# Kernel optimization log

Measured on AMD Instinct MI355X. Metric: run time of the kernel, lower is better.

Reference implementation:

```python
import jax, jax.numpy as jnp
import numpy as np

N = 100000      # nodes
E = 1600000     # edges (before self-loops)
IN = 128        # in_size
H = 4           # heads
C = 32          # out_size // heads
OUT = H * C     # 128
NEG_SLOPE = 0.2
LN_EPS = 1e-5
SM_EPS = 1e-16  # PyG softmax eps


def setup_inputs() -> dict:
    key = jax.random.key(0)
    ks = jax.random.split(key, 6)
    x = jax.random.normal(ks[0], (N, IN), dtype=jnp.float32)
    edge_index = jax.random.randint(ks[1], (2, E), 0, N, dtype=jnp.int64)
    W = jax.random.normal(ks[2], (IN, OUT), dtype=jnp.float32) * 0.05
    a_src = jax.random.normal(ks[3], (H, C), dtype=jnp.float32) * 0.05
    a_dst = jax.random.normal(ks[4], (H, C), dtype=jnp.float32) * 0.05
    bias = jnp.zeros((OUT,), dtype=jnp.float32)
    gamma = jnp.ones((OUT,), dtype=jnp.float32)
    beta = jnp.zeros((OUT,), dtype=jnp.float32)
    return {"x": x, "edge_index": edge_index, "W": W, "a_src": a_src,
            "a_dst": a_dst, "bias": bias, "gamma": gamma, "beta": beta}


def reference(x, edge_index, W, a_src, a_dst, bias, gamma, beta):
    n = x.shape[0]
    # add self loops (PyG GATConv default)
    loops = jnp.arange(n, dtype=edge_index.dtype)
    src = jnp.concatenate([edge_index[0], loops])  # [E+N]
    dst = jnp.concatenate([edge_index[1], loops])

    h = (x @ W).reshape(n, H, C)                   # [N,H,C]
    alpha_src = jnp.sum(h * a_src, axis=-1)        # [N,H]
    alpha_dst = jnp.sum(h * a_dst, axis=-1)        # [N,H]

    e = jax.nn.leaky_relu(alpha_src[src] + alpha_dst[dst], NEG_SLOPE)  # [E+N,H]
    # segment softmax over edges grouped by destination node
    emax = jax.ops.segment_max(e, dst, num_segments=n)
    emax = jnp.where(jnp.isfinite(emax), emax, 0.0)
    ee = jnp.exp(e - emax[dst])
    denom = jax.ops.segment_sum(ee, dst, num_segments=n)
    alpha = ee / (denom[dst] + SM_EPS)             # [E+N,H]

    msg = h[src] * alpha[:, :, None]               # [E+N,H,C]
    out = jax.ops.segment_sum(msg, dst, num_segments=n).reshape(n, OUT) + bias

    # LayerNorm(out_size)
    mu = jnp.mean(out, axis=-1, keepdims=True)
    var = jnp.var(out, axis=-1, keepdims=True)
    out = (out - mu) * jax.lax.rsqrt(var + LN_EPS) * gamma + beta
    return jax.nn.relu(out)
```

## Files before the change

### kernel.cpp

```cpp
#include <hip/hip_runtime.h>
#include <hip/hip_bf16.h>
#include <math.h>

#define IN_DIM 128
#define OUT_DIM 128
#define NHEAD 4
#define HC 32
#define NEG_SLOPE 0.2f
#define LN_EPS 1e-5f
#define SM_EPS 1e-16f

#define NB_SHIFT 9
#define BDST 512
#define NBUCK_MAX 256
#define BIN_ITER 28
#define BIN_CHUNK (BIN_ITER * 256)
#define SRC_BITS 17
#define SRC_MASK ((1u << SRC_BITS) - 1u)
#define BCAP_SHIFT 14
#define BCAP (1 << BCAP_SHIFT)

typedef __attribute__((ext_vector_type(8))) short bf16x8;
typedef __attribute__((ext_vector_type(4))) short short4v;
typedef __attribute__((ext_vector_type(4))) float f32x4;

__device__ __forceinline__ float leaky(float v) { return v > 0.f ? v : NEG_SLOPE * v; }

__device__ __forceinline__ short f2b(float f) {
    __hip_bfloat16 b = __float2bfloat16(f);
    return *reinterpret_cast<short*>(&b);
}
__device__ __forceinline__ float b2f(short s) {
    return __uint_as_float(((unsigned)(unsigned short)s) << 16);
}

__device__ __forceinline__ int swz(int row, int byteInRow) {
    return row * 256 + (byteInRow ^ ((row & 7) << 4));
}

__global__ void k_prepW(const float* __restrict__ W, __hip_bfloat16* __restrict__ WtB,
                        int* __restrict__ bcur)
{
    int t0 = blockIdx.x * 256 + threadIdx.x;
    int k = t0 >> 7, j = t0 & 127;
    WtB[j * IN_DIM + k] = __float2bfloat16(W[t0]);
    if (blockIdx.x == 0) bcur[threadIdx.x] = 0;
}

__global__ void __launch_bounds__(256)
k_gemm_bin(const float* __restrict__ x, const __hip_bfloat16* __restrict__ WtB,
           const float* __restrict__ a_src, const float* __restrict__ a_dst,
           __hip_bfloat16* __restrict__ hB, float* __restrict__ asrc_out,
           float* __restrict__ adst_out,
           const int* __restrict__ ei, int* __restrict__ bcur,
           unsigned* __restrict__ binned,
           int E, int N, int nblk_bin)
{
    __shared__ __align__(16) char lds[32768];
    const int t = threadIdx.x;

    if ((int)blockIdx.x < nblk_bin) {
        int* cnt = (int*)lds;
        int* gb  = (int*)(lds + 1024);
        int tot = E + N;
        int base = (int)blockIdx.x * BIN_CHUNK;

        cnt[t] = 0;
        __syncthreads();

        int rk[BIN_ITER], bk[BIN_ITER], dlo[BIN_ITER];
        #pragma unroll
        for (int k = 0; k < BIN_ITER; ++k) {
            int e = base + k * 256 + t;
            bk[k] = -1; rk[k] = 0; dlo[k] = 0;
            if (e < tot) {
                int d = (e < E) ? ei[E + e] : (e - E);
                bk[k] = d >> NB_SHIFT;
                dlo[k] = d & (BDST - 1);
                rk[k] = atomicAdd(&cnt[bk[k]], 1);
            }
        }
        __syncthreads();
        gb[t] = cnt[t] ? ((t << BCAP_SHIFT) + atomicAdd(&bcur[t], cnt[t])) : 0;
        __syncthreads();
        #pragma unroll
        for (int k = 0; k < BIN_ITER; ++k) {
            int e = base + k * 256 + t;
            if (e < tot) {
                int s = (e < E) ? ei[e] : (e - E);
                binned[gb[bk[k]] + rk[k]] = (unsigned)s | ((unsigned)dlo[k] << SRC_BITS);
            }
        }
    } else {
        const int node0 = ((int)blockIdx.x - nblk_bin) * 64;

        #pragma unroll
        for (int i = 0; i < 16; ++i) {
            int idx = (i * 256 + t) * 4;
            int col = idx >> 7, k = idx & 127;
            short4v w4 = *reinterpret_cast<const short4v*>((const short*)WtB + idx);
            *reinterpret_cast<short4v*>(lds + swz(col, 2 * k)) = w4;
        }

        const int wave = t >> 6, l = t & 63;
        const int lr = l & 15, lg = l >> 4;

        int arow = node0 + wave * 16 + lr;
        bf16x8 afrag[4];
        if (arow < N) {
            const float* xr = x + (size_t)arow * IN_DIM + lg * 8;
            #pragma unroll
            for (int kk = 0; kk < 4; ++kk) {
                float4 xa = *reinterpret_cast<const float4*>(xr + kk * 32);
                float4 xc = *reinterpret_cast<const float4*>(xr + kk * 32 + 4);
                afrag[kk] = (bf16x8){ f2b(xa.x), f2b(xa.y), f2b(xa.z), f2b(xa.w),
                                      f2b(xc.x), f2b(xc.y), f2b(xc.z), f2b(xc.w) };
            }
        } else {
            #pragma unroll
            for (int kk = 0; kk < 4; ++kk)
                afrag[kk] = (bf16x8){0,0,0,0,0,0,0,0};
        }

        __syncthreads();

        f32x4 acc[8];
        #pragma unroll
        for (int cg = 0; cg < 8; ++cg) acc[cg] = (f32x4){0.f, 0.f, 0.f, 0.f};

        #pragma unroll
        for (int cg = 0; cg < 8; ++cg) {
            #pragma unroll
            for (int kk = 0; kk < 4; ++kk) {
                bf16x8 b = *reinterpret_cast<bf16x8*>(lds + swz(cg * 16 + lr, kk * 64 + lg * 16));
                acc[cg] = __builtin_amdgcn_mfma_f32_16x16x32_bf16(afrag[kk], b, acc[cg], 0, 0, 0);
            }
        }

        __syncthreads();
        #pragma unroll
        for (int q = 0; q < 4; ++q) {
            int row = wave * 16 + lg * 4 + q;
            #pragma unroll
            for (int cg = 0; cg < 8; ++cg)
                *reinterpret_cast<short*>(lds + swz(row, (cg * 16 + lr) * 2)) = f2b(acc[cg][q]);
        }
        __syncthreads();

        {
            int row = t >> 2;
            int node = node0 + row;
            int head = t & 3;
            if (node < N) {
                char* dst = (char*)(hB + (size_t)node * OUT_DIM);
                const float4* asv = (const float4*)(a_src + head * HC);
                const float4* adv = (const float4*)(a_dst + head * HC);
                float s = 0.f, dd = 0.f;
                #pragma unroll
                for (int c = 0; c < 4; ++c) {
                    int bir = head * 64 + c * 16;
                    bf16x8 vv = *reinterpret_cast<bf16x8*>(lds + swz(row, bir));
                    *reinterpret_cast<bf16x8*>(dst + bir) = vv;
                    float4 a0 = asv[c * 2], a1 = asv[c * 2 + 1];
                    float4 d0 = adv[c * 2], d1 = adv[c * 2 + 1];
                    s  = fmaf(b2f(vv[0]), a0.x, s);  dd = fmaf(b2f(vv[0]), d0.x, dd);
                    s  = fmaf(b2f(vv[1]), a0.y, s);  dd = fmaf(b2f(vv[1]), d0.y, dd);
                    s  = fmaf(b2f(vv[2]), a0.z, s);  dd = fmaf(b2f(vv[2]), d0.z, dd);
                    s  = fmaf(b2f(vv[3]), a0.w, s);  dd = fmaf(b2f(vv[3]), d0.w, dd);
                    s  = fmaf(b2f(vv[4]), a1.x, s);  dd = fmaf(b2f(vv[4]), d1.x, dd);
                    s  = fmaf(b2f(vv[5]), a1.y, s);  dd = fmaf(b2f(vv[5]), d1.y, dd);
                    s  = fmaf(b2f(vv[6]), a1.z, s);  dd = fmaf(b2f(vv[6]), d1.z, dd);
                    s  = fmaf(b2f(vv[7]), a1.w, s);  dd = fmaf(b2f(vv[7]), d1.w, dd);
                }
                asrc_out[node * NHEAD + head] = s;
                adst_out[node * NHEAD + head] = dd;
            }
        }
    }
}

__global__ void k_bucket_csr(const unsigned* __restrict__ binned, const int* __restrict__ bcur,
                             int* __restrict__ rowbeg, int* __restrict__ rowend,
                             int* __restrict__ csr_src, int N)
{
    __shared__ int cnt[BDST];
    __shared__ int s2[256];
    int b = blockIdx.x;
    int t = threadIdx.x;
    int d0 = b << NB_SHIFT;
    int base = b << BCAP_SHIFT;
    int ne = bcur[b];

    cnt[t] = 0; cnt[t + 256] = 0;
    __syncthreads();
    for (int i = t; i < ne; i += 256) {
        unsigned p = binned[base + i];
        atomicAdd(&cnt[p >> SRC_BITS], 1);
    }
    __syncthreads();
    int c0 = cnt[2 * t], c1 = cnt[2 * t + 1];
    s2[t] = c0 + c1;
    __syncthreads();
    #pragma unroll
    for (int off = 1; off < 256; off <<= 1) {
        int tmp = (t >= off) ? s2[t - off] : 0;
        __syncthreads();
        s2[t] += tmp;
        __syncthreads();
    }
    int e0 = (t ? s2[t - 1] : 0);
    cnt[2 * t] = e0;
    cnt[2 * t + 1] = e0 + c0;
    if (d0 + 2 * t < N) {
        rowbeg[d0 + 2 * t] = base + e0;
        rowend[d0 + 2 * t] = base + e0 + c0;
    }
    if (d0 + 2 * t + 1 < N) {
        rowbeg[d0 + 2 * t + 1] = base + e0 + c0;
        rowend[d0 + 2 * t + 1] = base + e0 + c0 + c1;
    }
    __syncthreads();
    for (int i = t; i < ne; i += 256) {
        unsigned p = binned[base + i];
        int r = atomicAdd(&cnt[p >> SRC_BITS], 1);
        csr_src[base + r] = (int)(p & SRC_MASK);
    }
}

__global__ void k_gather(const int* __restrict__ csr_src,
                         const int* __restrict__ rowbeg, const int* __restrict__ rowend,
                         const __hip_bfloat16* __restrict__ hB,
                         const float* __restrict__ asrc, const float* __restrict__ adst,
                         const float* __restrict__ bias, const float* __restrict__ gamma,
                         const float* __restrict__ beta, float* __restrict__ out, int N)
{
    int wave = threadIdx.x >> 6;
    int l = threadIdx.x & 63;
    int d = blockIdx.x * 4 + wave;
    if (d >= N) return;
    int head = l >> 4;
    const char* hp = (const char*)hB;
    unsigned voff = (unsigned)(l << 2);
    float ad = adst[d * NHEAD + head];
    int beg = __builtin_amdgcn_readfirstlane(rowbeg[d]);
    int end = __builtin_amdgcn_readfirstlane(rowend[d]);

    float ax0 = 0.f, ay0 = 0.f, dn0 = 0.f;
    float ax1 = 0.f, ay1 = 0.f, dn1 = 0.f;

    int idx = beg + (l & 15);
    int cl = idx < end ? idx : end - 1;
    int smine = csr_src[cl];
    float v = (idx < end) ? asrc[(unsigned)smine * NHEAD + head] : -1e30f;

    for (int c = beg; c < end; c += 16) {
        float ee = __expf(leaky(v + ad));
        int scur = smine;
        int c2 = c + 16;
        if (c2 < end) {
            int idx2 = c2 + (l & 15);
            int cl2 = idx2 < end ? idx2 : end - 1;
            smine = csr_src[cl2];
            v = (idx2 < end) ? asrc[(unsigned)smine * NHEAD + head] : -1e30f;
        }

#define GLOAD(E_)                                                                     \
        unsigned se##E_ = (unsigned)__builtin_amdgcn_readlane(scur, (E_));            \
        unsigned hv##E_ = *(const unsigned*)(hp + ((se##E_ << 8) + voff));
#define GCONS(E_, AX_, AY_, DN_) {                                                    \
        float eb = __int_as_float(__builtin_amdgcn_ds_swizzle(                        \
            __float_as_int(ee), 0x10 | ((E_) << 5)));                                 \
        AX_ = fmaf(eb, __uint_as_float(hv##E_ << 16), AX_);                           \
        AY_ = fmaf(eb, __uint_as_float(hv##E_ & 0xffff0000u), AY_);  DN_ += eb;       \
    }
        { GLOAD(0) GLOAD(1) GLOAD(2) GLOAD(3) GLOAD(4) GLOAD(5) GLOAD(6) GLOAD(7)
          GCONS(0, ax0, ay0, dn0) GCONS(1, ax1, ay1, dn1)
          GCONS(2, ax0, ay0, dn0) GCONS(3, ax1, ay1, dn1)
          GCONS(4, ax0, ay0, dn0) GCONS(5, ax1, ay1, dn1)
          GCONS(6, ax0, ay0, dn0) GCONS(7, ax1, ay1, dn1) }
        { GLOAD(8) GLOAD(9) GLOAD(10) GLOAD(11) GLOAD(12) GLOAD(13) GLOAD(14) GLOAD(15)
          GCONS(8, ax0, ay0, dn0)  GCONS(9, ax1, ay1, dn1)
          GCONS(10, ax0, ay0, dn0) GCONS(11, ax1, ay1, dn1)
          GCONS(12, ax0, ay0, dn0) GCONS(13, ax1, ay1, dn1)
          GCONS(14, ax0, ay0, dn0) GCONS(15, ax1, ay1, dn1) }
#undef GLOAD
#undef GCONS
    }

    float accx = ax0 + ax1, accy = ay0 + ay1, den = dn0 + dn1;
    float inv = 1.f / (den + SM_EPS);
    float vx = accx * inv + bias[2 * l];
    float vy = accy * inv + bias[2 * l + 1];

    float s1 = vx + vy;
    float s2 = vx * vx + vy * vy;
    #pragma unroll
    for (int m = 32; m >= 1; m >>= 1) {
        s1 += __shfl_xor(s1, m, 64);
        s2 += __shfl_xor(s2, m, 64);
    }
    float mean = s1 * (1.f / OUT_DIM);
    float var = s2 * (1.f / OUT_DIM) - mean * mean;
    float r = rsqrtf(var + LN_EPS);
    float ox = (vx - mean) * r * gamma[2 * l] + beta[2 * l];
    float oy = (vy - mean) * r * gamma[2 * l + 1] + beta[2 * l + 1];
    ox = ox > 0.f ? ox : 0.f;
    oy = oy > 0.f ? oy : 0.f;
    *reinterpret_cast<float2*>(&out[(size_t)d * OUT_DIM + 2 * l]) = make_float2(ox, oy);
}

extern "C" void kernel_launch(void* const* d_in, const int* in_sizes, int n_in,
                              void* d_out, int out_size, void* d_ws, size_t ws_size,
                              hipStream_t stream) {
    const float* x      = (const float*)d_in[0];
    const int*   ei     = (const int*)d_in[1];
    const float* W      = (const float*)d_in[2];
    const float* a_src  = (const float*)d_in[3];
    const float* a_dst  = (const float*)d_in[4];
    const float* bias   = (const float*)d_in[5];
    const float* gamma  = (const float*)d_in[6];
    const float* beta   = (const float*)d_in[7];
    float* out = (float*)d_out;

    const int N = in_sizes[0] / IN_DIM;
    const int E = in_sizes[1] / 2;
    const int TOT = E + N;
    const int nbuck = (N + BDST - 1) >> NB_SHIFT;
    const int nblk_gemm = (N + 63) / 64;
    const int nblk_bin = (TOT + BIN_CHUNK - 1) / BIN_CHUNK;

    char* p = (char*)d_ws;
    __hip_bfloat16* hB = (__hip_bfloat16*)p;  p += (size_t)N * OUT_DIM * sizeof(__hip_bfloat16);
    __hip_bfloat16* WtB = (__hip_bfloat16*)p; p += (size_t)IN_DIM * OUT_DIM * sizeof(__hip_bfloat16);
    float* asrc   = (float*)p;                p += (size_t)N * NHEAD * sizeof(float);
    float* adst   = (float*)p;                p += (size_t)N * NHEAD * sizeof(float);
    int* bcur     = (int*)p;                  p += NBUCK_MAX * sizeof(int);
    int* rowbeg   = (int*)p;                  p += (size_t)N * sizeof(int);
    int* rowend   = (int*)p;                  p += (size_t)N * sizeof(int);
    unsigned* binned = (unsigned*)p;          p += (size_t)nbuck * BCAP * sizeof(unsigned);
    int* csr_src  = (int*)p;                  p += (size_t)nbuck * BCAP * sizeof(int);

    k_prepW<<<64, 256, 0, stream>>>(W, WtB, bcur);
    k_gemm_bin<<<nblk_bin + nblk_gemm, 256, 0, stream>>>(x, WtB, a_src, a_dst, hB, asrc, adst,
                                                         ei, bcur, binned, E, N, nblk_bin);
    k_bucket_csr<<<nbuck, 256, 0, stream>>>(binned, bcur, rowbeg, rowend, csr_src, N);
    k_gather<<<(N + 3) / 4, 256, 0, stream>>>(csr_src, rowbeg, rowend, hB, asrc, adst,
                                              bias, gamma, beta, out, N);
}
```

Baseline: 152.8 us.

## Regroup stages: bin edges with W prep, fuse CSR build with GEMM

Edge binning now runs in the same launch as the W transpose/convert, and the per-bucket CSR construction shares a launch with the node GEMM. The old bucket-CSR kernel is removed and the bcur reset moves to a memset. The aim is to overlap independent work across stages and cut one serialized launch. In exchange, binning now reads destination indices twice instead of keeping ranks in registers, and the memset adds a small extra operation.

```diff
diff --git a/kernel.cpp b/kernel.cpp
--- a/kernel.cpp
+++ b/kernel.cpp
@@ -38,61 +38,108 @@
     return row * 256 + (byteInRow ^ ((row & 7) << 4));
 }
 
-__global__ void k_prepW(const float* __restrict__ W, __hip_bfloat16* __restrict__ WtB,
-                        int* __restrict__ bcur)
+__global__ void __launch_bounds__(256)
+k_bin_prep(const int* __restrict__ ei, int* __restrict__ bcur, unsigned* __restrict__ binned,
+           const float* __restrict__ W, __hip_bfloat16* __restrict__ WtB,
+           int E, int N, int nblk_bin)
 {
-    int t0 = blockIdx.x * 256 + threadIdx.x;
-    int k = t0 >> 7, j = t0 & 127;
-    WtB[j * IN_DIM + k] = __float2bfloat16(W[t0]);
-    if (blockIdx.x == 0) bcur[threadIdx.x] = 0;
+    __shared__ int cnt[NBUCK_MAX];
+    __shared__ int gb[NBUCK_MAX];
+    __shared__ int cnt2[NBUCK_MAX];
+    const int t = threadIdx.x;
+
+    if ((int)blockIdx.x < nblk_bin) {
+        int tot = E + N;
+        int base = (int)blockIdx.x * BIN_CHUNK;
+
+        cnt[t] = 0;
+        __syncthreads();
+        #pragma unroll 4
+        for (int k = 0; k < BIN_ITER; ++k) {
+            int e = base + k * 256 + t;
+            if (e < tot) {
+                int d = (e < E) ? ei[E + e] : (e - E);
+                atomicAdd(&cnt[d >> NB_SHIFT], 1);
+            }
+        }
+        __syncthreads();
+        gb[t] = cnt[t] ? ((t << BCAP_SHIFT) + atomicAdd(&bcur[t], cnt[t])) : 0;
+        cnt2[t] = 0;
+        __syncthreads();
+        #pragma unroll 4
+        for (int k = 0; k < BIN_ITER; ++k) {
+            int e = base + k * 256 + t;
+            if (e < tot) {
+                int d = (e < E) ? ei[E + e] : (e - E);
+                int b = d >> NB_SHIFT;
+                int r = atomicAdd(&cnt2[b], 1);
+                int s = (e < E) ? ei[e] : (e - E);
+                binned[gb[b] + r] = (unsigned)s | ((unsigned)(d & (BDST - 1)) << SRC_BITS);
+            }
+        }
+    } else {
+        int t0 = ((int)blockIdx.x - nblk_bin) * 256 + t;
+        int k = t0 >> 7, j = t0 & 127;
+        WtB[j * IN_DIM + k] = __float2bfloat16(W[t0]);
+    }
 }
 
 __global__ void __launch_bounds__(256)
-k_gemm_bin(const float* __restrict__ x, const __hip_bfloat16* __restrict__ WtB,
+k_csr_gemm(const unsigned* __restrict__ binned, const int* __restrict__ bcur,
+           int* __restrict__ rowbeg, int* __restrict__ rowend, int* __restrict__ csr_src,
+           const float* __restrict__ x, const __hip_bfloat16* __restrict__ WtB,
            const float* __restrict__ a_src, const float* __restrict__ a_dst,
            __hip_bfloat16* __restrict__ hB, float* __restrict__ asrc_out,
            float* __restrict__ adst_out,
-           const int* __restrict__ ei, int* __restrict__ bcur,
-           unsigned* __restrict__ binned,
-           int E, int N, int nblk_bin)
+           int N, int nbuck)
 {
     __shared__ __align__(16) char lds[32768];
     const int t = threadIdx.x;
 
-    if ((int)blockIdx.x < nblk_bin) {
+    if ((int)blockIdx.x < nbuck) {
         int* cnt = (int*)lds;
-        int* gb  = (int*)(lds + 1024);
-        int tot = E + N;
-        int base = (int)blockIdx.x * BIN_CHUNK;
-
-        cnt[t] = 0;
-        __syncthreads();
-
-        int rk[BIN_ITER], bk[BIN_ITER], dlo[BIN_ITER];
-        #pragma unroll
-        for (int k = 0; k < BIN_ITER; ++k) {
-            int e = base + k * 256 + t;
-            bk[k] = -1; rk[k] = 0; dlo[k] = 0;
-            if (e < tot) {
-                int d = (e < E) ? ei[E + e] : (e - E);
-                bk[k] = d >> NB_SHIFT;
-                dlo[k] = d & (BDST - 1);
-                rk[k] = atomicAdd(&cnt[bk[k]], 1);
-            }
-        }
-        __syncthreads();
-        gb[t] = cnt[t] ? ((t << BCAP_SHIFT) + atomicAdd(&bcur[t], cnt[t])) : 0;
-        __syncthreads();
-        #pragma unroll
-        for (int k = 0; k < BIN_ITER; ++k) {
-            int e = base + k * 256 + t;
-            if (e < tot) {
-                int s = (e < E) ? ei[e] : (e - E);
-                binned[gb[bk[k]] + rk[k]] = (unsigned)s | ((unsigned)dlo[k] << SRC_BITS);
-            }
+        int* s2  = (int*)(lds + BDST * 4);
+        int b = blockIdx.x;
+        int d0 = b << NB_SHIFT;
+        int base = b << BCAP_SHIFT;
+        int ne = bcur[b];
+
+        cnt[t] = 0; cnt[t + 256] = 0;
+        __syncthreads();
+        for (int i = t; i < ne; i += 256) {
+            unsigned p = binned[base + i];
+            atomicAdd(&cnt[p >> SRC_BITS], 1);
+        }
+        __syncthreads();
+        int c0 = cnt[2 * t], c1 = cnt[2 * t + 1];
+        s2[t] = c0 + c1;
+        __syncthreads();
+        #pragma unroll
+        for (int off = 1; off < 256; off <<= 1) {
+            int tmp = (t >= off) ? s2[t - off] : 0;
+            __syncthreads();
+            s2[t] += tmp;
+            __syncthreads();
+        }
+        int e0 = (t ? s2[t - 1] : 0);
+        cnt[2 * t] = e0;
+        cnt[2 * t + 1] = e0 + c0;
+        if (d0 + 2 * t < N) {
+            rowbeg[d0 + 2 * t] = base + e0;
+            rowend[d0 + 2 * t] = base + e0 + c0;
+        }
+        if (d0 + 2 * t + 1 < N) {
+            rowbeg[d0 + 2 * t + 1] = base + e0 + c0;
+            rowend[d0 + 2 * t + 1] = base + e0 + c0 + c1;
+        }
+        __syncthreads();
+        for (int i = t; i < ne; i += 256) {
+            unsigned p = binned[base + i];
+            int r = atomicAdd(&cnt[p >> SRC_BITS], 1);
+            csr_src[base + r] = (int)(p & SRC_MASK);
         }
     } else {
-        const int node0 = ((int)blockIdx.x - nblk_bin) * 64;
+        const int node0 = ((int)blockIdx.x - nbuck) * 64;
 
         #pragma unroll
         for (int i = 0; i < 16; ++i) {
@@ -179,54 +226,6 @@
     }
 }
 
-__global__ void k_bucket_csr(const unsigned* __restrict__ binned, const int* __restrict__ bcur,
-                             int* __restrict__ rowbeg, int* __restrict__ rowend,
-                             int* __restrict__ csr_src, int N)
-{
-    __shared__ int cnt[BDST];
-    __shared__ int s2[256];
-    int b = blockIdx.x;
-    int t = threadIdx.x;
-    int d0 = b << NB_SHIFT;
-    int base = b << BCAP_SHIFT;
-    int ne = bcur[b];
-
-    cnt[t] = 0; cnt[t + 256] = 0;
-    __syncthreads();
-    for (int i = t; i < ne; i += 256) {
-        unsigned p = binned[base + i];
-        atomicAdd(&cnt[p >> SRC_BITS], 1);
-    }
-    __syncthreads();
-    int c0 = cnt[2 * t], c1 = cnt[2 * t + 1];
-    s2[t] = c0 + c1;
-    __syncthreads();
-    #pragma unroll
-    for (int off = 1; off < 256; off <<= 1) {
-        int tmp = (t >= off) ? s2[t - off] : 0;
-        __syncthreads();
-        s2[t] += tmp;
-        __syncthreads();
-    }
-    int e0 = (t ? s2[t - 1] : 0);
-    cnt[2 * t] = e0;
-    cnt[2 * t + 1] = e0 + c0;
-    if (d0 + 2 * t < N) {
-        rowbeg[d0 + 2 * t] = base + e0;
-        rowend[d0 + 2 * t] = base + e0 + c0;
-    }
-    if (d0 + 2 * t + 1 < N) {
-        rowbeg[d0 + 2 * t + 1] = base + e0 + c0;
-        rowend[d0 + 2 * t + 1] = base + e0 + c0 + c1;
-    }
-    __syncthreads();
-    for (int i = t; i < ne; i += 256) {
-        unsigned p = binned[base + i];
-        int r = atomicAdd(&cnt[p >> SRC_BITS], 1);
-        csr_src[base + r] = (int)(p & SRC_MASK);
-    }
-}
-
 __global__ void k_gather(const int* __restrict__ csr_src,
                          const int* __restrict__ rowbeg, const int* __restrict__ rowend,
                          const __hip_bfloat16* __restrict__ hB,
@@ -340,10 +339,12 @@
     unsigned* binned = (unsigned*)p;          p += (size_t)nbuck * BCAP * sizeof(unsigned);
     int* csr_src  = (int*)p;                  p += (size_t)nbuck * BCAP * sizeof(int);
 
-    k_prepW<<<64, 256, 0, stream>>>(W, WtB, bcur);
-    k_gemm_bin<<<nblk_bin + nblk_gemm, 256, 0, stream>>>(x, WtB, a_src, a_dst, hB, asrc, adst,
-                                                         ei, bcur, binned, E, N, nblk_bin);
-    k_bucket_csr<<<nbuck, 256, 0, stream>>>(binned, bcur, rowbeg, rowend, csr_src, N);
+    (void)hipMemsetAsync(bcur, 0, NBUCK_MAX * sizeof(int), stream);
+
+    k_bin_prep<<<nblk_bin + 64, 256, 0, stream>>>(ei, bcur, binned, W, WtB, E, N, nblk_bin);
+    k_csr_gemm<<<nbuck + nblk_gemm, 256, 0, stream>>>(binned, bcur, rowbeg, rowend, csr_src,
+                                                      x, WtB, a_src, a_dst, hB, asrc, adst,
+                                                      N, nbuck);
     k_gather<<<(N + 3) / 4, 256, 0, stream>>>(csr_src, rowbeg, rowend, hB, asrc, adst,
                                               bias, gamma, beta, out, N);
 }
```

Measured after the change: 159.7 us. 4.5% more time.
